# Performance work log

Measured on AMD Instinct MI355X. Metric: run time of the kernel, lower is better.

## Reference

```python
import jax, jax.numpy as jnp
import numpy as np

ALPHA = 0.2  # LeakyReLU negative slope
B, L, FIN, FOUT = 128, 512, 128, 128

def setup_inputs() -> dict:
    key = jax.random.key(0)
    k1, k2, k3, k4, k5 = jax.random.split(key, 5)
    h = jax.random.normal(k1, (B, L, FIN), jnp.float32)
    W = jax.random.normal(k2, (FIN, FOUT), jnp.float32) * (1.0 / np.sqrt(FIN))
    a = jax.random.normal(k3, (2 * FOUT,), jnp.float32) * (1.0 / np.sqrt(2 * FOUT))
    edge_bias = jax.random.normal(k4, (B, L, L), jnp.float32) * 0.1
    adj_mask = jax.random.uniform(k5, (L, L)) > 0.3
    adj_mask = adj_mask | jnp.eye(L, dtype=bool)  # self-loops avoid fully-masked rows
    return {"h": h, "W": W, "a": a, "edge_bias": edge_bias, "adj_mask": adj_mask}

def reference(h, W, a, edge_bias, adj_mask):
    # Wh: [B, L, Fout]
    Wh = jnp.einsum('blf,fo->blo', h, W)
    Fout = W.shape[1]
    # a([Wh_i, Wh_j]) == Wh_i @ a[:Fout] + Wh_j @ a[Fout:]  (avoids O(B*L*L*2F) concat)
    ei = Wh @ a[:Fout]   # [B, L]  (target i contribution)
    ej = Wh @ a[Fout:]   # [B, L]  (source j contribution)
    e = jax.nn.leaky_relu(ei[:, :, None] + ej[:, None, :], ALPHA) + edge_bias  # [B, L, L]
    e = jnp.where(adj_mask[None, :, :], e, -jnp.inf)
    att = jax.nn.softmax(e, axis=-1)  # dropout=0.0 -> identity
    h_prime = jnp.einsum('bij,bjo->bio', att, Wh)  # [B, L, Fout]
    return jax.nn.elu(h_prime)  # concat=True branch
```

## Files before the change

### kernel.cpp

```cpp
#include <hip/hip_runtime.h>
#include <string.h>

#define ALPHA 0.2f

typedef short short8 __attribute__((ext_vector_type(8)));
typedef float floatx4 __attribute__((ext_vector_type(4)));
typedef int intx4 __attribute__((ext_vector_type(4)));
typedef unsigned short ushort4v __attribute__((ext_vector_type(4)));

__device__ inline unsigned short f2bf(float f) {
    unsigned int v; __builtin_memcpy(&v, &f, 4);
    v = v + 0x7FFFu + ((v >> 16) & 1u);
    return (unsigned short)(v >> 16);
}

__device__ inline floatx4 ntload_f4(const float* p) {
    return __builtin_nontemporal_load((const floatx4*)p);
}

__global__ __launch_bounds__(256) void mask_kernel(const int* __restrict__ adj,
                                                   unsigned long long* __restrict__ mask)
{
    const int lane = threadIdx.x & 63;
    const int wv   = threadIdx.x >> 6;
    const int row  = blockIdx.x * 4 + wv;
    const int* ar  = adj + row * 512;
    unsigned long long w0, w1, w2, w3, w4, w5, w6, w7;
    w0 = __ballot(ar[0 * 64 + lane] != 0);
    w1 = __ballot(ar[1 * 64 + lane] != 0);
    w2 = __ballot(ar[2 * 64 + lane] != 0);
    w3 = __ballot(ar[3 * 64 + lane] != 0);
    w4 = __ballot(ar[4 * 64 + lane] != 0);
    w5 = __ballot(ar[5 * 64 + lane] != 0);
    w6 = __ballot(ar[6 * 64 + lane] != 0);
    w7 = __ballot(ar[7 * 64 + lane] != 0);
    if (lane == 0) {
        unsigned long long* mr = mask + row * 8;
        mr[0] = w0; mr[1] = w1; mr[2] = w2; mr[3] = w3;
        mr[4] = w4; mr[5] = w5; mr[6] = w6; mr[7] = w7;
    }
}

__global__ __launch_bounds__(256) void wh_kernel(const float* __restrict__ h,
                                                 const float* __restrict__ W,
                                                 const float* __restrict__ a,
                                                 unsigned short* __restrict__ wht,
                                                 float* __restrict__ ei,
                                                 float* __restrict__ ej)
{
    __shared__ __align__(16) unsigned short h_s[128][136];
    __shared__ __align__(16) unsigned short w_s[128][136];
    __shared__ float a_s[256];
    const int tid  = threadIdx.x;
    const int lane = tid & 63;
    const int wv   = tid >> 6;
    const int quad = lane >> 4;
    const int l16  = lane & 15;
    const int r0   = blockIdx.x * 128;
    const int b    = r0 >> 9;
    const int jb   = r0 & 511;

    const float* hbase = h + (size_t)r0 * 128;
    for (int it = 0; it < 16; ++it) {
        int idx4 = it * 256 + tid;
        floatx4 v = *(const floatx4*)(hbase + idx4 * 4);
        int row = idx4 >> 5;
        int col = (idx4 & 31) * 4;
        ushort4v u;
        for (int e = 0; e < 4; ++e) u[e] = f2bf(v[e]);
        *(ushort4v*)&h_s[row][col] = u;
    }
    for (int it = 0; it < 64; ++it) {
        int idx = it * 256 + tid;
        w_s[idx & 127][idx >> 7] = f2bf(W[idx]);
    }
    a_s[tid] = a[tid];
    __syncthreads();

    floatx4 acc[8][2];
    for (int mo = 0; mo < 8; ++mo)
        for (int n = 0; n < 2; ++n) acc[mo][n] = (floatx4)0.f;

    for (int kk = 0; kk < 4; ++kk) {
        short8 bfr[2];
        for (int n = 0; n < 2; ++n)
            bfr[n] = *(const short8*)&h_s[wv * 32 + n * 16 + l16][kk * 32 + quad * 8];
        for (int mo = 0; mo < 8; ++mo) {
            short8 afr = *(const short8*)&w_s[mo * 16 + l16][kk * 32 + quad * 8];
            acc[mo][0] = __builtin_amdgcn_mfma_f32_16x16x32_bf16(afr, bfr[0], acc[mo][0], 0, 0, 0);
            acc[mo][1] = __builtin_amdgcn_mfma_f32_16x16x32_bf16(afr, bfr[1], acc[mo][1], 0, 0, 0);
        }
    }

    for (int n = 0; n < 2; ++n) {
        float si = 0.f, sj = 0.f;
        for (int mo = 0; mo < 8; ++mo)
            for (int r = 0; r < 4; ++r) {
                int o = mo * 16 + quad * 4 + r;
                float v = acc[mo][n][r];
                si += v * a_s[o];
                sj += v * a_s[128 + o];
            }
        si += __shfl_xor(si, 16); si += __shfl_xor(si, 32);
        sj += __shfl_xor(sj, 16); sj += __shfl_xor(sj, 32);
        if (quad == 0) {
            int j = jb + wv * 32 + n * 16 + l16;
            ei[b * 512 + j] = si;
            ej[b * 512 + j] = sj;
        }
    }

    for (int mo = 0; mo < 8; ++mo)
        for (int n = 0; n < 2; ++n)
            for (int r = 0; r < 4; ++r) {
                int o = mo * 16 + quad * 4 + r;
                int j = jb + wv * 32 + n * 16 + l16;
                wht[(size_t)b * 65536 + o * 512 + j] = f2bf(acc[mo][n][r]);
            }
}

__global__ __launch_bounds__(512, 4) void attn_kernel(const unsigned short* __restrict__ wht,
                                                      const float* __restrict__ ei,
                                                      const float* __restrict__ ej,
                                                      const float* __restrict__ bias,
                                                      const unsigned* __restrict__ mask32,
                                                      float* __restrict__ out)
{
    __shared__ __align__(16) unsigned short p_s[64][520];
    __shared__ float ei_s[64];
    __shared__ float s_row[64];

    const int tid  = threadIdx.x;
    const int lane = tid & 63;
    const int wv   = tid >> 6;
    const int quad = lane >> 4;
    const int l16  = lane & 15;

    const int n  = blockIdx.x;
    const int x  = n & 7;
    const int r  = n >> 3;
    const int b  = x * 16 + (r >> 3);
    const int i0 = (r & 7) * 64;

    const float*    bp = bias + ((size_t)(b * 512 + i0 + wv * 8)) * 512;
    const unsigned* mp = mask32 + (i0 + wv * 8) * 16;
    const int mw = lane >> 3;
    const int ms = (lane & 7) * 4;
    floatx4 bb0 = ntload_f4(bp + lane * 4);
    floatx4 bb1 = ntload_f4(bp + 256 + lane * 4);
    unsigned cm0 = mp[mw];
    unsigned cm1 = mp[8 + mw];

    const floatx4 ejv0 = *(const floatx4*)(ej + b * 512 + lane * 4);
    const floatx4 ejv1 = *(const floatx4*)(ej + b * 512 + 256 + lane * 4);
    if (tid < 64) ei_s[tid] = ei[b * 512 + i0 + tid];
    __syncthreads();

    float rsum[8];

#pragma unroll
    for (int rr = 0; rr < 8; ++rr) {
        floatx4 nb0, nb1; unsigned nm0, nm1;
        if (rr < 7) {
            nb0 = ntload_f4(bp + 512 + lane * 4);
            nb1 = ntload_f4(bp + 768 + lane * 4);
            nm0 = mp[16 + mw];
            nm1 = mp[24 + mw];
        }
        const int il = wv * 8 + rr;
        const float eiv = ei_s[il];
        const unsigned nib0 = (cm0 >> ms) & 0xFu;
        const unsigned nib1 = (cm1 >> ms) & 0xFu;
        float sm = 0.f;
        ushort4v p0, p1;
#pragma unroll
        for (int e = 0; e < 4; ++e) {
            float xv = eiv + ejv0[e];
            xv = fmaxf(xv, ALPHA * xv);
            xv += bb0[e];
            float p = __expf(xv);
            p = (nib0 & (1u << e)) ? p : 0.f;
            sm += p;
            p0[e] = f2bf(p);
        }
#pragma unroll
        for (int e = 0; e < 4; ++e) {
            float xv = eiv + ejv1[e];
            xv = fmaxf(xv, ALPHA * xv);
            xv += bb1[e];
            float p = __expf(xv);
            p = (nib1 & (1u << e)) ? p : 0.f;
            sm += p;
            p1[e] = f2bf(p);
        }
        *(ushort4v*)&p_s[il][lane * 4]       = p0;
        *(ushort4v*)&p_s[il][256 + lane * 4] = p1;
        rsum[rr] = sm;
        bb0 = nb0; bb1 = nb1; cm0 = nm0; cm1 = nm1;
        bp += 512; mp += 16;
    }

#pragma unroll
    for (int rr = 0; rr < 8; ++rr)
        for (int off = 32; off; off >>= 1)
            rsum[rr] += __shfl_xor(rsum[rr], off);
    if (lane == 0)
#pragma unroll
        for (int rr = 0; rr < 8; ++rr) s_row[wv * 8 + rr] = rsum[rr];
    __syncthreads();

    floatx4 acc[4];
#pragma unroll
    for (int m = 0; m < 4; ++m) acc[m] = (floatx4)0.f;

    const unsigned short* wb = wht + (size_t)b * 65536 + (wv * 16 + l16) * 512 + quad * 8;
    short8 bf = *(const short8*)(wb);
#pragma unroll
    for (int k16 = 0; k16 < 16; ++k16) {
        int ko = k16 * 32 + quad * 8;
        short8 nbf;
        if (k16 < 15) nbf = *(const short8*)(wb + (k16 + 1) * 32);
        short8 af0 = *(const short8*)&p_s[l16][ko];
        short8 af1 = *(const short8*)&p_s[16 + l16][ko];
        short8 af2 = *(const short8*)&p_s[32 + l16][ko];
        short8 af3 = *(const short8*)&p_s[48 + l16][ko];
        acc[0] = __builtin_amdgcn_mfma_f32_16x16x32_bf16(af0, bf, acc[0], 0, 0, 0);
        acc[1] = __builtin_amdgcn_mfma_f32_16x16x32_bf16(af1, bf, acc[1], 0, 0, 0);
        acc[2] = __builtin_amdgcn_mfma_f32_16x16x32_bf16(af2, bf, acc[2], 0, 0, 0);
        acc[3] = __builtin_amdgcn_mfma_f32_16x16x32_bf16(af3, bf, acc[3], 0, 0, 0);
        bf = nbf;
    }

#pragma unroll
    for (int m = 0; m < 4; ++m)
#pragma unroll
        for (int rr2 = 0; rr2 < 4; ++rr2) {
            int il = m * 16 + quad * 4 + rr2;
            int o  = wv * 16 + l16;
            float v = acc[m][rr2] / s_row[il];
            v = v > 0.f ? v : (__expf(v) - 1.f);
            __builtin_nontemporal_store(v, &out[((size_t)(b * 512 + i0 + il)) * 128 + o]);
        }
}

extern "C" void kernel_launch(void* const* d_in, const int* in_sizes, int n_in,
                              void* d_out, int out_size, void* d_ws, size_t ws_size,
                              hipStream_t stream)
{
    const float* h    = (const float*)d_in[0];
    const float* W    = (const float*)d_in[1];
    const float* a    = (const float*)d_in[2];
    const float* bias = (const float*)d_in[3];
    const int*   adj  = (const int*)d_in[4];
    float*       out  = (float*)d_out;

    unsigned short* wht = (unsigned short*)d_ws;
    float* ei = (float*)((char*)d_ws + 16777216);
    float* ej = ei + 65536;
    unsigned long long* mask = (unsigned long long*)((char*)d_ws + 17301504);

    hipLaunchKernelGGL(mask_kernel, dim3(128),  dim3(256), 0, stream, adj, mask);
    hipLaunchKernelGGL(wh_kernel,   dim3(512),  dim3(256), 0, stream, h, W, a, wht, ei, ej);
    hipLaunchKernelGGL(attn_kernel, dim3(1024), dim3(512), 0, stream, wht, ei, ej, bias,
                       (const unsigned*)mask, out);
}
```

Measured before the change: 247.4 us.

## Fuse mask into Wh kernel, load h directly, process two row tiles per attention block

Folds the adjacency-mask bit-packing into the Wh GEMM kernel, removing one launch. The Wh kernel now converts h to bf16 straight from global memory into registers with prefetch instead of staging it in shared memory. The attention kernel handles two 64-row tiles per block on half the grid, prefetching bias and mask for the second tile during the first tile's MFMA phase. This adds register pressure and a serial second pass in each block.

Measured after the change: 245.4 us. No clear change (-0.8%).

```diff
diff --git a/kernel.cpp b/kernel.cpp
--- a/kernel.cpp
+++ b/kernel.cpp
@@ -5,7 +5,6 @@
 
 typedef short short8 __attribute__((ext_vector_type(8)));
 typedef float floatx4 __attribute__((ext_vector_type(4)));
-typedef int intx4 __attribute__((ext_vector_type(4)));
 typedef unsigned short ushort4v __attribute__((ext_vector_type(4)));
 
 __device__ inline unsigned short f2bf(float f) {
@@ -18,37 +17,15 @@
     return __builtin_nontemporal_load((const floatx4*)p);
 }
 
-__global__ __launch_bounds__(256) void mask_kernel(const int* __restrict__ adj,
-                                                   unsigned long long* __restrict__ mask)
+__global__ __launch_bounds__(256, 4) void wh_kernel(const float* __restrict__ h,
+                                                    const float* __restrict__ W,
+                                                    const float* __restrict__ a,
+                                                    const int* __restrict__ adj,
+                                                    unsigned short* __restrict__ wht,
+                                                    float* __restrict__ ei,
+                                                    float* __restrict__ ej,
+                                                    unsigned long long* __restrict__ mask)
 {
-    const int lane = threadIdx.x & 63;
-    const int wv   = threadIdx.x >> 6;
-    const int row  = blockIdx.x * 4 + wv;
-    const int* ar  = adj + row * 512;
-    unsigned long long w0, w1, w2, w3, w4, w5, w6, w7;
-    w0 = __ballot(ar[0 * 64 + lane] != 0);
-    w1 = __ballot(ar[1 * 64 + lane] != 0);
-    w2 = __ballot(ar[2 * 64 + lane] != 0);
-    w3 = __ballot(ar[3 * 64 + lane] != 0);
-    w4 = __ballot(ar[4 * 64 + lane] != 0);
-    w5 = __ballot(ar[5 * 64 + lane] != 0);
-    w6 = __ballot(ar[6 * 64 + lane] != 0);
-    w7 = __ballot(ar[7 * 64 + lane] != 0);
-    if (lane == 0) {
-        unsigned long long* mr = mask + row * 8;
-        mr[0] = w0; mr[1] = w1; mr[2] = w2; mr[3] = w3;
-        mr[4] = w4; mr[5] = w5; mr[6] = w6; mr[7] = w7;
-    }
-}
-
-__global__ __launch_bounds__(256) void wh_kernel(const float* __restrict__ h,
-                                                 const float* __restrict__ W,
-                                                 const float* __restrict__ a,
-                                                 unsigned short* __restrict__ wht,
-                                                 float* __restrict__ ei,
-                                                 float* __restrict__ ej)
-{
-    __shared__ __align__(16) unsigned short h_s[128][136];
     __shared__ __align__(16) unsigned short w_s[128][136];
     __shared__ float a_s[256];
     const int tid  = threadIdx.x;
@@ -60,36 +37,61 @@
     const int b    = r0 >> 9;
     const int jb   = r0 & 511;
 
-    const float* hbase = h + (size_t)r0 * 128;
-    for (int it = 0; it < 16; ++it) {
-        int idx4 = it * 256 + tid;
-        floatx4 v = *(const floatx4*)(hbase + idx4 * 4);
-        int row = idx4 >> 5;
-        int col = (idx4 & 31) * 4;
-        ushort4v u;
-        for (int e = 0; e < 4; ++e) u[e] = f2bf(v[e]);
-        *(ushort4v*)&h_s[row][col] = u;
-    }
     for (int it = 0; it < 64; ++it) {
         int idx = it * 256 + tid;
         w_s[idx & 127][idx >> 7] = f2bf(W[idx]);
     }
     a_s[tid] = a[tid];
-    __syncthreads();
+
+    if (blockIdx.x < 128) {
+        const int row = blockIdx.x * 4 + wv;
+        const int* ar = adj + row * 512;
+        unsigned long long wbits[8];
+#pragma unroll
+        for (int q = 0; q < 8; ++q) wbits[q] = __ballot(ar[q * 64 + lane] != 0);
+        if (lane == 0) {
+            unsigned long long* mr = mask + row * 8;
+#pragma unroll
+            for (int q = 0; q < 8; ++q) mr[q] = wbits[q];
+        }
+    }
+    __syncthreads();
+
+    const float* hp0 = h + (size_t)(r0 + wv * 32 + l16) * 128 + quad * 8;
+    const float* hp1 = hp0 + 16 * 128;
 
     floatx4 acc[8][2];
     for (int mo = 0; mo < 8; ++mo)
         for (int n = 0; n < 2; ++n) acc[mo][n] = (floatx4)0.f;
 
+    floatx4 c00 = *(const floatx4*)(hp0);
+    floatx4 c01 = *(const floatx4*)(hp0 + 4);
+    floatx4 c10 = *(const floatx4*)(hp1);
+    floatx4 c11 = *(const floatx4*)(hp1 + 4);
+#pragma unroll
     for (int kk = 0; kk < 4; ++kk) {
-        short8 bfr[2];
-        for (int n = 0; n < 2; ++n)
-            bfr[n] = *(const short8*)&h_s[wv * 32 + n * 16 + l16][kk * 32 + quad * 8];
+        floatx4 n00, n01, n10, n11;
+        if (kk < 3) {
+            n00 = *(const floatx4*)(hp0 + (kk + 1) * 32);
+            n01 = *(const floatx4*)(hp0 + (kk + 1) * 32 + 4);
+            n10 = *(const floatx4*)(hp1 + (kk + 1) * 32);
+            n11 = *(const floatx4*)(hp1 + (kk + 1) * 32 + 4);
+        }
+        short8 bfr0, bfr1;
+#pragma unroll
+        for (int e = 0; e < 4; ++e) {
+            bfr0[e]     = (short)f2bf(c00[e]);
+            bfr0[4 + e] = (short)f2bf(c01[e]);
+            bfr1[e]     = (short)f2bf(c10[e]);
+            bfr1[4 + e] = (short)f2bf(c11[e]);
+        }
+#pragma unroll
         for (int mo = 0; mo < 8; ++mo) {
             short8 afr = *(const short8*)&w_s[mo * 16 + l16][kk * 32 + quad * 8];
-            acc[mo][0] = __builtin_amdgcn_mfma_f32_16x16x32_bf16(afr, bfr[0], acc[mo][0], 0, 0, 0);
-            acc[mo][1] = __builtin_amdgcn_mfma_f32_16x16x32_bf16(afr, bfr[1], acc[mo][1], 0, 0, 0);
-        }
+            acc[mo][0] = __builtin_amdgcn_mfma_f32_16x16x32_bf16(afr, bfr0, acc[mo][0], 0, 0, 0);
+            acc[mo][1] = __builtin_amdgcn_mfma_f32_16x16x32_bf16(afr, bfr1, acc[mo][1], 0, 0, 0);
+        }
+        c00 = n00; c01 = n01; c10 = n10; c11 = n11;
     }
 
     for (int n = 0; n < 2; ++n) {
@@ -127,7 +129,7 @@
                                                       float* __restrict__ out)
 {
     __shared__ __align__(16) unsigned short p_s[64][520];
-    __shared__ float ei_s[64];
+    __shared__ float ei_s[2][64];
     __shared__ float s_row[64];
 
     const int tid  = threadIdx.x;
@@ -136,16 +138,19 @@
     const int quad = lane >> 4;
     const int l16  = lane & 15;
 
-    const int n  = blockIdx.x;
-    const int x  = n & 7;
-    const int r  = n >> 3;
-    const int b  = x * 16 + (r >> 3);
-    const int i0 = (r & 7) * 64;
+    const int x  = blockIdx.x & 7;
+    const int r2 = blockIdx.x >> 3;
+    const int bl = r2 >> 2;
+    const int tp = r2 & 3;
+    const int b  = x * 16 + bl;
+    const int i0 = (tp * 2) * 64;
+    const int i1 = i0 + 64;
+
+    const int mw = lane >> 3;
+    const int ms = (lane & 7) * 4;
 
     const float*    bp = bias + ((size_t)(b * 512 + i0 + wv * 8)) * 512;
     const unsigned* mp = mask32 + (i0 + wv * 8) * 16;
-    const int mw = lane >> 3;
-    const int ms = (lane & 7) * 4;
     floatx4 bb0 = ntload_f4(bp + lane * 4);
     floatx4 bb1 = ntload_f4(bp + 256 + lane * 4);
     unsigned cm0 = mp[mw];
@@ -153,7 +158,8 @@
 
     const floatx4 ejv0 = *(const floatx4*)(ej + b * 512 + lane * 4);
     const floatx4 ejv1 = *(const floatx4*)(ej + b * 512 + 256 + lane * 4);
-    if (tid < 64) ei_s[tid] = ei[b * 512 + i0 + tid];
+    if (tid < 64) ei_s[0][tid] = ei[b * 512 + i0 + tid];
+    else if (tid < 128) ei_s[1][tid - 64] = ei[b * 512 + i1 + (tid - 64)];
     __syncthreads();
 
     float rsum[8];
@@ -168,7 +174,7 @@
             nm1 = mp[24 + mw];
         }
         const int il = wv * 8 + rr;
-        const float eiv = ei_s[il];
+        const float eiv = ei_s[0][il];
         const unsigned nib0 = (cm0 >> ms) & 0xFu;
         const unsigned nib1 = (cm1 >> ms) & 0xFu;
         float sm = 0.f;
@@ -208,6 +214,17 @@
 #pragma unroll
         for (int rr = 0; rr < 8; ++rr) s_row[wv * 8 + rr] = rsum[rr];
     __syncthreads();
+
+    const float*    bp1 = bias + ((size_t)(b * 512 + i1 + wv * 8)) * 512;
+    const unsigned* mp1 = mask32 + (i1 + wv * 8) * 16;
+    floatx4 q0[4], q1[4]; unsigned qm0[4], qm1[4];
+#pragma unroll
+    for (int rr = 0; rr < 4; ++rr) {
+        q0[rr]  = ntload_f4(bp1 + (size_t)rr * 512 + lane * 4);
+        q1[rr]  = ntload_f4(bp1 + (size_t)rr * 512 + 256 + lane * 4);
+        qm0[rr] = mp1[rr * 16 + mw];
+        qm1[rr] = mp1[rr * 16 + 8 + mw];
+    }
 
     floatx4 acc[4];
 #pragma unroll
@@ -241,6 +258,89 @@
             v = v > 0.f ? v : (__expf(v) - 1.f);
             __builtin_nontemporal_store(v, &out[((size_t)(b * 512 + i0 + il)) * 128 + o]);
         }
+    __syncthreads();
+
+#pragma unroll
+    for (int rr = 0; rr < 8; ++rr) {
+        const int s = rr & 3;
+        floatx4 cb0 = q0[s], cb1 = q1[s];
+        unsigned m0 = qm0[s], m1 = qm1[s];
+        if (rr < 4) {
+            q0[s]  = ntload_f4(bp1 + (size_t)(rr + 4) * 512 + lane * 4);
+            q1[s]  = ntload_f4(bp1 + (size_t)(rr + 4) * 512 + 256 + lane * 4);
+            qm0[s] = mp1[(rr + 4) * 16 + mw];
+            qm1[s] = mp1[(rr + 4) * 16 + 8 + mw];
+        }
+        const int il = wv * 8 + rr;
+        const float eiv = ei_s[1][il];
+        const unsigned nib0 = (m0 >> ms) & 0xFu;
+        const unsigned nib1 = (m1 >> ms) & 0xFu;
+        float sm = 0.f;
+        ushort4v p0, p1;
+#pragma unroll
+        for (int e = 0; e < 4; ++e) {
+            float xv = eiv + ejv0[e];
+            xv = fmaxf(xv, ALPHA * xv);
+            xv += cb0[e];
+            float p = __expf(xv);
+            p = (nib0 & (1u << e)) ? p : 0.f;
+            sm += p;
+            p0[e] = f2bf(p);
+        }
+#pragma unroll
+        for (int e = 0; e < 4; ++e) {
+            float xv = eiv + ejv1[e];
+            xv = fmaxf(xv, ALPHA * xv);
+            xv += cb1[e];
+            float p = __expf(xv);
+            p = (nib1 & (1u << e)) ? p : 0.f;
+            sm += p;
+            p1[e] = f2bf(p);
+        }
+        *(ushort4v*)&p_s[il][lane * 4]       = p0;
+        *(ushort4v*)&p_s[il][256 + lane * 4] = p1;
+        rsum[rr] = sm;
+    }
+
+#pragma unroll
+    for (int rr = 0; rr < 8; ++rr)
+        for (int off = 32; off; off >>= 1)
+            rsum[rr] += __shfl_xor(rsum[rr], off);
+    if (lane == 0)
+#pragma unroll
+        for (int rr = 0; rr < 8; ++rr) s_row[wv * 8 + rr] = rsum[rr];
+    __syncthreads();
+
+#pragma unroll
+    for (int m = 0; m < 4; ++m) acc[m] = (floatx4)0.f;
+
+    bf = *(const short8*)(wb);
+#pragma unroll
+    for (int k16 = 0; k16 < 16; ++k16) {
+        int ko = k16 * 32 + quad * 8;
+        short8 nbf;
+        if (k16 < 15) nbf = *(const short8*)(wb + (k16 + 1) * 32);
+        short8 af0 = *(const short8*)&p_s[l16][ko];
+        short8 af1 = *(const short8*)&p_s[16 + l16][ko];
+        short8 af2 = *(const short8*)&p_s[32 + l16][ko];
+        short8 af3 = *(const short8*)&p_s[48 + l16][ko];
+        acc[0] = __builtin_amdgcn_mfma_f32_16x16x32_bf16(af0, bf, acc[0], 0, 0, 0);
+        acc[1] = __builtin_amdgcn_mfma_f32_16x16x32_bf16(af1, bf, acc[1], 0, 0, 0);
+        acc[2] = __builtin_amdgcn_mfma_f32_16x16x32_bf16(af2, bf, acc[2], 0, 0, 0);
+        acc[3] = __builtin_amdgcn_mfma_f32_16x16x32_bf16(af3, bf, acc[3], 0, 0, 0);
+        bf = nbf;
+    }
+
+#pragma unroll
+    for (int m = 0; m < 4; ++m)
+#pragma unroll
+        for (int rr2 = 0; rr2 < 4; ++rr2) {
+            int il = m * 16 + quad * 4 + rr2;
+            int o  = wv * 16 + l16;
+            float v = acc[m][rr2] / s_row[il];
+            v = v > 0.f ? v : (__expf(v) - 1.f);
+            __builtin_nontemporal_store(v, &out[((size_t)(b * 512 + i1 + il)) * 128 + o]);
+        }
 }
 
 extern "C" void kernel_launch(void* const* d_in, const int* in_sizes, int n_in,
@@ -259,8 +359,7 @@
     float* ej = ei + 65536;
     unsigned long long* mask = (unsigned long long*)((char*)d_ws + 17301504);
 
-    hipLaunchKernelGGL(mask_kernel, dim3(128),  dim3(256), 0, stream, adj, mask);
-    hipLaunchKernelGGL(wh_kernel,   dim3(512),  dim3(256), 0, stream, h, W, a, wht, ei, ej);
-    hipLaunchKernelGGL(attn_kernel, dim3(1024), dim3(512), 0, stream, wht, ei, ej, bias,
+    hipLaunchKernelGGL(wh_kernel,   dim3(512), dim3(256), 0, stream, h, W, a, adj, wht, ei, ej, mask);
+    hipLaunchKernelGGL(attn_kernel, dim3(512), dim3(512), 0, stream, wht, ei, ej, bias,
                        (const unsigned*)mask, out);
 }
```
